# Optimization experiments

Measured on AMD Instinct MI355X. Metric: run time of the kernel, lower is better.

The kernel has to match this reference:

```python
import math
import jax, jax.numpy as jnp
import numpy as np

B, H, L = 8, 512, 4096
N = 64 // 2  # d_state//2 complex pairs
DT_MIN, DT_MAX = 1e-3, 0.1


def setup_inputs() -> dict:
    key = jax.random.key(0)
    k_u, k_dt, k_C, k_D, k_W = jax.random.split(key, 5)
    u = jax.random.normal(k_u, (B, H, L), dtype=jnp.float32)
    log_dt = jax.random.uniform(k_dt, (H,), dtype=jnp.float32) * (
        math.log(DT_MAX) - math.log(DT_MIN)) + math.log(DT_MIN)
    log_A_real = jnp.log(0.5 * jnp.ones((H, N), dtype=jnp.float32))
    A_imag = math.pi * jnp.broadcast_to(jnp.arange(N, dtype=jnp.float32), (H, N))
    C = jax.random.normal(k_C, (H, N, 2), dtype=jnp.float32)  # view_as_real of cfloat
    D = jax.random.normal(k_D, (H,), dtype=jnp.float32)
    W_out = jax.random.normal(k_W, (2 * H, H), dtype=jnp.float32) * 0.05  # 1x1 conv weight
    b_out = jnp.zeros((2 * H,), dtype=jnp.float32)
    return {"u": u, "log_dt": log_dt, "log_A_real": log_A_real, "A_imag": A_imag,
            "C": C, "D": D, "W_out": W_out, "b_out": b_out}


def _ssm_kernel(log_dt, log_A_real, A_imag, C, length):
    dt = jnp.exp(log_dt)                             # (H,)
    A = -jnp.exp(log_A_real) + 1j * A_imag           # (H,N) complex
    dtA = A * dt[:, None]                            # (H,N)
    l = jnp.arange(length, dtype=jnp.float32)
    K = jnp.exp(dtA[:, :, None] * l)                 # (H,N,L) complex Vandermonde
    Cc = C[..., 0] + 1j * C[..., 1]                  # (H,N)
    Cs = Cc * (jnp.exp(dtA) - 1.0) / A               # (H,N)
    return 2.0 * jnp.einsum('hn,hnl->hl', Cs, K).real  # (H,L) real kernel


def reference(u, log_dt, log_A_real, A_imag, C, D, W_out, b_out):
    length = u.shape[-1]
    k = _ssm_kernel(log_dt, log_A_real, A_imag, C, length)  # (H,L)
    n_fft = 2 * length
    k_f = jnp.fft.rfft(k, n=n_fft)                   # (H, L+1)
    u_f = jnp.fft.rfft(u, n=n_fft)                   # (B,H,L+1)
    y = jnp.fft.irfft(u_f * k_f, n=n_fft)[..., :length]  # FFT convolution
    y = y + u * D[:, None]                           # D skip connection
    y = jax.nn.gelu(y, approximate=False)            # torch nn.GELU = exact erf
    y = jnp.einsum('oh,bhl->bol', W_out, y) + b_out[:, None]  # 1x1 conv
    a, b = jnp.split(y, 2, axis=-2)                  # GLU over channel dim
    return a * jax.nn.sigmoid(b)
```

## Files before the change

kernel.cpp:

```cpp
#include <hip/hip_runtime.h>
#include <math.h>

constexpr int cB = 8, cH = 512, cL = 4096, cN = 32;
constexpr int cG = 32, cLC = 128;
constexpr int cHN = cH * cN;

constexpr size_t OF_RR  = 0;
constexpr size_t OF_RI  = (size_t)cHN;
constexpr size_t OF_RPR = (size_t)2*cHN;
constexpr size_t OF_RPI = (size_t)3*cHN;
constexpr size_t OF_C2R = (size_t)4*cHN;
constexpr size_t OF_C2I = (size_t)5*cHN;
constexpr size_t OF_DR  = (size_t)6*cHN;
constexpr size_t OF_DI  = (size_t)7*cHN;
constexpr size_t OF_K   = (size_t)8*cHN;
constexpr size_t OF_WP  = OF_K + (size_t)512*128;
constexpr size_t OF_A   = OF_WP + (size_t)1024*512/2;
constexpr size_t OF_V   = OF_A + (size_t)512*128*192/2;
constexpr size_t OF_XP  = OF_V + (size_t)512*64*128/2;
constexpr size_t OF_G   = OF_XP + (size_t)512*256*64/2;
constexpr size_t OF_GT  = OF_A;

typedef __bf16 bf16x8 __attribute__((ext_vector_type(8)));
typedef float  f32x4  __attribute__((ext_vector_type(4)));

static __device__ __forceinline__ ushort f2bf(float x) {
    unsigned u = __float_as_uint(x);
    unsigned r = (u + 0x7fffu + ((u >> 16) & 1u)) >> 16;
    return (ushort)r;
}
static __device__ __forceinline__ float bf2f(ushort v) {
    return __uint_as_float(((unsigned)v) << 16);
}
static __device__ __forceinline__ unsigned pk2(float a, float b) {
    return (unsigned)f2bf(a) | ((unsigned)f2bf(b) << 16);
}
static __device__ __forceinline__ float gelu(float v) {
    return 0.5f * v * (1.0f + erff(v * 0.70710678118654752f));
}
static __device__ __forceinline__ void gload16(const void* g, void* l) {
    __builtin_amdgcn_global_load_lds(
        (const __attribute__((address_space(1))) unsigned*)g,
        (__attribute__((address_space(3))) unsigned*)l, 16, 0, 0);
}

__global__ void k_consts_vmat(const float* __restrict__ log_dt,
                              const float* __restrict__ log_A_real,
                              const float* __restrict__ A_imag,
                              const float* __restrict__ Cin,
                              float* __restrict__ ws,
                              ushort* __restrict__ wsu)
{
    int tid = blockIdx.x * 256 + threadIdx.x;
    if (tid >= cHN) return;
    int h = tid >> 5, n = tid & 31;
    float dt = expf(log_dt[h]);
    float Ar = -expf(log_A_real[tid]);
    float Ai = A_imag[tid];
    float dr = dt * Ar, di = dt * Ai;
    float er = expf(dr);
    float rr = er * cosf(di), ri = er * sinf(di);
    float erL = expf(dr * (float)cLC);
    float diL = di * (float)cLC;
    float rpr = erL * cosf(diL), rpi = erL * sinf(diL);
    float cr = Cin[2*tid], ci = Cin[2*tid+1];
    float nr = rr - 1.0f, ni = ri;
    float inv = 1.0f / (Ar*Ar + Ai*Ai);
    float wr = (nr*Ar + ni*Ai) * inv;
    float wi = (ni*Ar - nr*Ai) * inv;
    float csr = cr*wr - ci*wi;
    float csi = cr*wi + ci*wr;
    ws[OF_RR  + tid] = rr;  ws[OF_RI  + tid] = ri;
    ws[OF_RPR + tid] = rpr; ws[OF_RPI + tid] = rpi;
    ws[OF_C2R + tid] = 2.0f*csr; ws[OF_C2I + tid] = 2.0f*csi;
    ws[OF_DR  + tid] = dr;  ws[OF_DI  + tid] = di;

    float e127 = expf(dr * 127.f), a127 = di * 127.f;
    float pr = e127 * cosf(a127), pi_ = e127 * sinf(a127);
    float rie = expf(-dr);
    float rc = rie * cosf(di), rs = -rie * sinf(di);
    ushort* vre = wsu + 2*OF_V + ((size_t)h*64 + n) * 128;
    ushort* vim = wsu + 2*OF_V + ((size_t)h*64 + 32 + n) * 128;
    for (int j4 = 0; j4 < 128; j4 += 4) {
        ushort4 r4, i4;
        #pragma unroll
        for (int e = 0; e < 4; ++e) {
            ((ushort*)&r4)[e] = f2bf(pr);
            ((ushort*)&i4)[e] = f2bf(pi_);
            float npr = pr*rc - pi_*rs;
            float npi = pr*rs + pi_*rc;
            pr = npr; pi_ = npi;
        }
        *(ushort4*)&vre[j4] = r4;
        *(ushort4*)&vim[j4] = i4;
    }
}

__global__ void k_pack_w(const float* __restrict__ W, ushort* __restrict__ Wp)
{
    int idx = blockIdx.x * 256 + threadIdx.x;
    int base = idx * 4;
    int m = base >> 9;
    int k = base & 511;
    int src = (m & 1) ? (512 + (m >> 1)) : (m >> 1);
    float4 v = *(const float4*)&W[(size_t)src * 512 + k];
    ushort4 o;
    o.x = f2bf(v.x); o.y = f2bf(v.y); o.z = f2bf(v.z); o.w = f2bf(v.w);
    *(ushort4*)&Wp[base] = o;
}

__global__ void k_embt(const float* __restrict__ ws, const float* __restrict__ Dvec,
                       ushort* __restrict__ wsu)
{
    __shared__ float kv[256];
    int t = threadIdx.x;
    int tid = blockIdx.x * 256 + t;
    int h = tid >> 7, l = tid & 127;
    float fl = (float)l, fl1 = (float)(l + 1);
    const float* dr_ = ws + OF_DR + (size_t)h*32;
    const float* di_ = ws + OF_DI + (size_t)h*32;
    const float* c2r_ = ws + OF_C2R + (size_t)h*32;
    const float* c2i_ = ws + OF_C2I + (size_t)h*32;
    ushort* rowA = wsu + 2*OF_A + ((size_t)h*128 + l) * 192;
    float kacc = 0.f;
    for (int n4 = 0; n4 < 32; n4 += 4) {
        ushort4 prq, npq;
        #pragma unroll
        for (int e = 0; e < 4; ++e) {
            int n = n4 + e;
            float dr = dr_[n], di = di_[n], c2r = c2r_[n], c2i = c2i_[n];
            float e0 = expf(dr * fl), a0 = di * fl;
            float c0 = cosf(a0), s0 = sinf(a0);
            kacc += e0 * (c2r*c0 - c2i*s0);
            float e1 = expf(dr * fl1), a1 = di * fl1;
            float c1 = cosf(a1), s1 = sinf(a1);
            ((ushort*)&prq)[e] = f2bf(e1 * (c2r*c1 - c2i*s1));
            ((ushort*)&npq)[e] = f2bf(-e1 * (c2r*s1 + c2i*c1));
        }
        *(ushort4*)&rowA[128 + n4] = prq;
        *(ushort4*)&rowA[160 + n4] = npq;
    }
    kv[t] = kacc;
    __syncthreads();
    const float* krow = kv + ((t >> 7) << 7);
    float Dh = Dvec[h];
    for (int j8 = 0; j8 < 128; j8 += 8) {
        uint4 q;
        unsigned w[4];
        #pragma unroll
        for (int p = 0; p < 4; ++p) {
            int j0 = j8 + 2*p, j1 = j0 + 1;
            float v0 = (j0 <= l) ? krow[l - j0] : 0.f;
            float v1 = (j1 <= l) ? krow[l - j1] : 0.f;
            if (j0 == l) v0 += Dh;
            if (j1 == l) v1 += Dh;
            w[p] = pk2(v0, v1);
        }
        q.x = w[0]; q.y = w[1]; q.z = w[2]; q.w = w[3];
        *(uint4*)&rowA[j8] = q;
    }
}

__global__ __launch_bounds__(512) void k_conv(const float* __restrict__ u,
                                              const float* __restrict__ ws,
                                              const ushort* __restrict__ wsu,
                                              ushort* __restrict__ g)
{
    __shared__ ushort As[128 * 200];
    __shared__ ushort Bs[256 * 200];
    const int t = threadIdx.x;
    const int h = blockIdx.x;
    const int wave = t >> 6, lane = t & 63;
    const int wm = wave & 1, wn = wave >> 1;
    const int lm = lane & 15, q = lane >> 4;

    uint4 areg[6];
    const int arow = t >> 2, ac0 = (t & 3) * 48;
    {
        const ushort* Ab = wsu + 2*OF_A + ((size_t)h*128 + arow) * 192 + ac0;
        #pragma unroll
        for (int e = 0; e < 6; ++e) areg[e] = *(const uint4*)&Ab[8*e];
    }
    {
        const int vrow = t >> 3, vc0 = (t & 7) * 16;
        const ushort* vs = wsu + 2*OF_V + ((size_t)h*64 + vrow) * 128 + vc0;
        uint4 v0 = *(const uint4*)&vs[0], v1 = *(const uint4*)&vs[8];
        *(uint4*)&As[vrow*200 + vc0]     = v0;
        *(uint4*)&As[vrow*200 + vc0 + 8] = v1;
    }
    {
        const int gc = t >> 1, half = t & 1;
        const int ub = gc >> 5, uc = gc & 31;
        const float* up = u + ((size_t)(ub*cH + h)) * cL + (size_t)uc*128 + half*64;
        ushort* d = &Bs[gc * 200 + half*64];
        #pragma unroll
        for (int e = 0; e < 8; ++e) {
            float4 f0 = *(const float4*)&up[8*e];
            float4 f1 = *(const float4*)&up[8*e + 4];
            uint4 w;
            w.x = pk2(f0.x, f0.y); w.y = pk2(f0.z, f0.w);
            w.z = pk2(f1.x, f1.y); w.w = pk2(f1.z, f1.w);
            *(uint4*)&d[8*e] = w;
        }
    }
    __syncthreads();

    {
        f32x4 accs[4][2];
        #pragma unroll
        for (int i = 0; i < 4; ++i)
            #pragma unroll
            for (int j = 0; j < 2; ++j) accs[i][j] = (f32x4){0.f,0.f,0.f,0.f};
        #pragma unroll
        for (int j0 = 0; j0 < 128; j0 += 32) {
            bf16x8 vf[4], uf[2];
            #pragma unroll
            for (int mi = 0; mi < 4; ++mi)
                vf[mi] = *(const bf16x8*)&As[(16*mi + lm) * 200 + j0 + 8*q];
            #pragma unroll
            for (int ni = 0; ni < 2; ++ni)
                uf[ni] = *(const bf16x8*)&Bs[(32*wave + 16*ni + lm) * 200 + j0 + 8*q];
            #pragma unroll
            for (int mi = 0; mi < 4; ++mi)
                #pragma unroll
                for (int ni = 0; ni < 2; ++ni)
                    accs[mi][ni] = __builtin_amdgcn_mfma_f32_16x16x32_bf16(vf[mi], uf[ni], accs[mi][ni], 0,0,0);
        }
        #pragma unroll
        for (int mi = 0; mi < 4; ++mi)
            #pragma unroll
            for (int ni = 0; ni < 2; ++ni) {
                int col = 32*wave + 16*ni + lm;
                ushort4 st;
                st.x = f2bf(accs[mi][ni][0]); st.y = f2bf(accs[mi][ni][1]);
                st.z = f2bf(accs[mi][ni][2]); st.w = f2bf(accs[mi][ni][3]);
                *(ushort4*)&Bs[col*200 + 128 + 16*mi + 4*q] = st;
            }
    }
    __syncthreads();

    if (t < 256) {
        const int sb = t >> 5, sn = t & 31;
        float rpr = ws[OF_RPR + (size_t)h*32 + sn];
        float rpi = ws[OF_RPI + (size_t)h*32 + sn];
        float Xr = 0.f, Xi = 0.f;
        ushort* p = &Bs[(sb*32) * 200 + 128 + sn];
        #pragma unroll 4
        for (int c = 0; c < cG; ++c, p += 200) {
            float sr = bf2f(p[0]), si = bf2f(p[32]);
            p[0]  = f2bf(Xr);
            p[32] = f2bf(Xi);
            float nXr = fmaf(rpr, Xr, fmaf(-rpi, Xi, sr));
            float nXi = fmaf(rpr, Xi, fmaf(rpi, Xr, si));
            Xr = nXr; Xi = nXi;
        }
    }
    {
        ushort* d = &As[arow*200 + ac0];
        #pragma unroll
        for (int e = 0; e < 6; ++e) *(uint4*)&d[8*e] = areg[e];
    }
    __syncthreads();

    f32x4 acc[4][4];
    #pragma unroll
    for (int i = 0; i < 4; ++i)
        #pragma unroll
        for (int j = 0; j < 4; ++j) acc[i][j] = (f32x4){0.f,0.f,0.f,0.f};

    #pragma unroll
    for (int k0 = 0; k0 < 192; k0 += 32) {
        if ((wm == 0) && (k0 == 64 || k0 == 96)) continue;
        bf16x8 af[4], bfr[4];
        #pragma unroll
        for (int mi = 0; mi < 4; ++mi)
            af[mi] = *(const bf16x8*)&As[(64*wm + 16*mi + lm) * 200 + k0 + 8*q];
        #pragma unroll
        for (int ni = 0; ni < 4; ++ni)
            bfr[ni] = *(const bf16x8*)&Bs[(64*wn + 16*ni + lm) * 200 + k0 + 8*q];
        #pragma unroll
        for (int mi = 0; mi < 4; ++mi)
            #pragma unroll
            for (int ni = 0; ni < 4; ++ni)
                acc[mi][ni] = __builtin_amdgcn_mfma_f32_16x16x32_bf16(af[mi], bfr[ni], acc[mi][ni], 0,0,0);
    }
    #pragma unroll
    for (int ni = 0; ni < 4; ++ni) {
        int gc = 64*wn + 16*ni + lm;
        int ob = gc >> 5, oc = gc & 31;
        ushort* grow = g + ((size_t)(ob*cH + h)) * cL + (size_t)oc*128;
        #pragma unroll
        for (int mi = 0; mi < 4; ++mi) {
            int l = 64*wm + 16*mi + 4*q;
            ushort4 st;
            st.x = f2bf(gelu(acc[mi][ni][0]));
            st.y = f2bf(gelu(acc[mi][ni][1]));
            st.z = f2bf(gelu(acc[mi][ni][2]));
            st.w = f2bf(gelu(acc[mi][ni][3]));
            *(ushort4*)&grow[l] = st;
        }
    }
}

__global__ __launch_bounds__(256) void k_transpose(const ushort* __restrict__ gsrc,
                                                   ushort* __restrict__ gT)
{
    __shared__ ushort tile[64 * 64];
    const int t = threadIdx.x;
    const int b  = blockIdx.z;
    const int h0 = blockIdx.y << 6;
    const int l0 = blockIdx.x << 6;
    const ushort* gb = gsrc + ((size_t)b * cH + h0) * cL + l0;
    const int lb = t & 7;
    #pragma unroll
    for (int half = 0; half < 2; ++half) {
        int r = (t >> 3) + half * 32;
        uint4 v = *(const uint4*)&gb[(size_t)r * cL + lb * 8];
        int sb = lb ^ (r & 7) ^ (r >> 3);
        *(uint4*)&tile[r * 64 + sb * 8] = v;
    }
    __syncthreads();
    ushort* gTb = gT + ((size_t)b * cL + l0) * cH + h0;
    #pragma unroll
    for (int half = 0; half < 2; ++half) {
        int l  = (t >> 3) + half * 32;
        int hb = t & 7;
        ushort vals[8];
        #pragma unroll
        for (int e = 0; e < 8; ++e) {
            int r  = hb * 8 + e;
            int sb = (l >> 3) ^ (r & 7) ^ (r >> 3);
            vals[e] = tile[r * 64 + sb * 8 + (l & 7)];
        }
        *(uint4*)&gTb[(size_t)l * cH + hb * 8] = *(uint4*)vals;
    }
}

__global__ __launch_bounds__(256) void k_gemm2(const ushort* __restrict__ Wp,
                                               const float* __restrict__ bias,
                                               const ushort* __restrict__ gT,
                                               float* __restrict__ out)
{
    __shared__ ushort As[2][128 * 32];
    __shared__ ushort Bs[2][128 * 32];
    const int t    = threadIdx.x;
    const int l0   = blockIdx.x * 128;
    const int by   = blockIdx.y;
    const int b    = blockIdx.z;
    const int wave = t >> 6, lane = t & 63;
    const int wm   = wave & 1, wn = wave >> 1;
    const int lm   = lane & 15, q = lane >> 4;

    const int srow = lane >> 2;
    const int scol = (lane & 3) * 8;
    const ushort* Ag = Wp + (size_t)(by * 128) * 512;
    const ushort* Bg = gT + ((size_t)b * cL + l0) * 512;

    f32x4 acc[4][4];
    #pragma unroll
    for (int i = 0; i < 4; ++i)
        #pragma unroll
        for (int j = 0; j < 4; ++j)
            acc[i][j] = (f32x4){0.f, 0.f, 0.f, 0.f};

    auto stage = [&](ushort* Asb, ushort* Bsb, int k0) {
        #pragma unroll
        for (int j = 0; j < 2; ++j) {
            int row = 32*wave + 16*j + srow;
            gload16(Ag + (size_t)row * 512 + k0 + scol,
                    (char*)Asb + wave*2048 + j*1024);
            gload16(Bg + (size_t)row * 512 + k0 + scol,
                    (char*)Bsb + wave*2048 + j*1024);
        }
    };
    auto compute = [&](const ushort* Asb, const ushort* Bsb) {
        bf16x8 af[4], bfr[4];
        #pragma unroll
        for (int mi = 0; mi < 4; ++mi)
            af[mi] = *(const bf16x8*)&Asb[(64*wm + 16*mi + lm) * 32 + 8*q];
        #pragma unroll
        for (int ni = 0; ni < 4; ++ni)
            bfr[ni] = *(const bf16x8*)&Bsb[(64*wn + 16*ni + lm) * 32 + 8*q];
        #pragma unroll
        for (int mi = 0; mi < 4; ++mi)
            #pragma unroll
            for (int ni = 0; ni < 4; ++ni)
                acc[mi][ni] = __builtin_amdgcn_mfma_f32_16x16x32_bf16(af[mi], bfr[ni], acc[mi][ni], 0,0,0);
    };

    stage(As[0], Bs[0], 0);
    __syncthreads();
    int cur = 0;
    for (int ks = 0; ks < 15; ++ks) {
        stage(As[cur ^ 1], Bs[cur ^ 1], (ks + 1) * 32);
        compute(As[cur], Bs[cur]);
        __syncthreads();
        cur ^= 1;
    }
    compute(As[cur], Bs[cur]);

    const int obase = by * 64 + 32 * wm;
    #pragma unroll
    for (int mi = 0; mi < 4; ++mi) {
        #pragma unroll
        for (int p = 0; p < 2; ++p) {
            int o = obase + 8*mi + 2*q + p;
            float ba = bias[o], bb = bias[512 + o];
            float* orow = out + ((size_t)b * cH + o) * cL + l0 + 64*wn + lm;
            #pragma unroll
            for (int ni = 0; ni < 4; ++ni) {
                float av = acc[mi][ni][2*p]     + ba;
                float gv = acc[mi][ni][2*p + 1] + bb;
                orow[16 * ni] = av / (1.f + expf(-gv));
            }
        }
    }
}

extern "C" void kernel_launch(void* const* d_in, const int* in_sizes, int n_in,
                              void* d_out, int out_size, void* d_ws, size_t ws_size,
                              hipStream_t stream)
{
    (void)in_sizes; (void)n_in; (void)out_size; (void)ws_size;
    const float* u          = (const float*)d_in[0];
    const float* log_dt     = (const float*)d_in[1];
    const float* log_A_real = (const float*)d_in[2];
    const float* A_imag     = (const float*)d_in[3];
    const float* C          = (const float*)d_in[4];
    const float* D          = (const float*)d_in[5];
    const float* W          = (const float*)d_in[6];
    const float* bias       = (const float*)d_in[7];
    float* out = (float*)d_out;
    float* ws  = (float*)d_ws;
    ushort* wsu = (ushort*)d_ws;
    ushort* Wp  = wsu + 2*OF_WP;
    ushort* gbf = wsu + 2*OF_G;
    ushort* gTu = wsu + 2*OF_GT;

    hipLaunchKernelGGL(k_consts_vmat, dim3(cHN/256), dim3(256), 0, stream,
                       log_dt, log_A_real, A_imag, C, ws, wsu);
    hipLaunchKernelGGL(k_pack_w, dim3(1024*512/4/256), dim3(256), 0, stream, W, Wp);
    hipLaunchKernelGGL(k_embt, dim3(512*128/256), dim3(256), 0, stream, ws, D, wsu);
    hipLaunchKernelGGL(k_conv, dim3(512), dim3(512), 0, stream, u, ws, wsu, gbf);
    hipLaunchKernelGGL(k_transpose, dim3(cL/64, cH/64, cB), dim3(256), 0, stream, gbf, gTu);
    hipLaunchKernelGGL(k_gemm2, dim3(cL/128, 1024/128, cB), dim3(256), 0, stream,
                       Wp, bias, gTu, out);
}
```

Measured before the change: 267.2 us.

## Double k_conv block to 1024 threads and stage output through LDS

k_conv now runs 16 waves per block instead of 8, halving each wave's MFMA tile in both the intra-chunk GEMM and the chunk-output GEMM, and splitting the global loads across more threads. The GELU results are first written into a padded shared-memory tile and then stored to global memory as contiguous 16-byte vectors, replacing scattered 8-byte stores. This aims for more latency hiding and better-coalesced writes. It costs extra barriers, and the single block per CU (LDS at about 150KB) means one synchronisation stall can leave the whole CU idle.

```diff
diff --git a/kernel.cpp b/kernel.cpp
--- a/kernel.cpp
+++ b/kernel.cpp
@@ -161,40 +161,40 @@
     }
 }
 
-__global__ __launch_bounds__(512) void k_conv(const float* __restrict__ u,
-                                              const float* __restrict__ ws,
-                                              const ushort* __restrict__ wsu,
-                                              ushort* __restrict__ g)
-{
-    __shared__ ushort As[128 * 200];
-    __shared__ ushort Bs[256 * 200];
+__global__ __launch_bounds__(1024) void k_conv(const float* __restrict__ u,
+                                               const float* __restrict__ ws,
+                                               const ushort* __restrict__ wsu,
+                                               ushort* __restrict__ g)
+{
+    __shared__ ushort sh[76800];
+    ushort* As = sh;
+    ushort* Bs = sh + 25600;
+    ushort* Os = sh;
+
     const int t = threadIdx.x;
     const int h = blockIdx.x;
     const int wave = t >> 6, lane = t & 63;
-    const int wm = wave & 1, wn = wave >> 1;
     const int lm = lane & 15, q = lane >> 4;
 
-    uint4 areg[6];
-    const int arow = t >> 2, ac0 = (t & 3) * 48;
+    uint4 areg[3];
+    const int arow = t >> 3, ac0 = (t & 7) * 24;
     {
         const ushort* Ab = wsu + 2*OF_A + ((size_t)h*128 + arow) * 192 + ac0;
         #pragma unroll
-        for (int e = 0; e < 6; ++e) areg[e] = *(const uint4*)&Ab[8*e];
-    }
-    {
-        const int vrow = t >> 3, vc0 = (t & 7) * 16;
-        const ushort* vs = wsu + 2*OF_V + ((size_t)h*64 + vrow) * 128 + vc0;
-        uint4 v0 = *(const uint4*)&vs[0], v1 = *(const uint4*)&vs[8];
-        *(uint4*)&As[vrow*200 + vc0]     = v0;
-        *(uint4*)&As[vrow*200 + vc0 + 8] = v1;
-    }
-    {
-        const int gc = t >> 1, half = t & 1;
+        for (int e = 0; e < 3; ++e) areg[e] = *(const uint4*)&Ab[8*e];
+    }
+    {
+        const int vrow = t >> 4, vc0 = (t & 15) * 8;
+        *(uint4*)&As[vrow*200 + vc0] =
+            *(const uint4*)(wsu + 2*OF_V + ((size_t)h*64 + vrow) * 128 + vc0);
+    }
+    {
+        const int gc = t >> 2, qt = t & 3;
         const int ub = gc >> 5, uc = gc & 31;
-        const float* up = u + ((size_t)(ub*cH + h)) * cL + (size_t)uc*128 + half*64;
-        ushort* d = &Bs[gc * 200 + half*64];
-        #pragma unroll
-        for (int e = 0; e < 8; ++e) {
+        const float* up = u + ((size_t)(ub*cH + h)) * cL + (size_t)uc*128 + qt*32;
+        ushort* d = &Bs[gc * 200 + qt*32];
+        #pragma unroll
+        for (int e = 0; e < 4; ++e) {
             float4 f0 = *(const float4*)&up[8*e];
             float4 f1 = *(const float4*)&up[8*e + 4];
             uint4 w;
@@ -206,36 +206,28 @@
     __syncthreads();
 
     {
-        f32x4 accs[4][2];
-        #pragma unroll
-        for (int i = 0; i < 4; ++i)
-            #pragma unroll
-            for (int j = 0; j < 2; ++j) accs[i][j] = (f32x4){0.f,0.f,0.f,0.f};
+        f32x4 accs[4];
+        #pragma unroll
+        for (int i = 0; i < 4; ++i) accs[i] = (f32x4){0.f,0.f,0.f,0.f};
         #pragma unroll
         for (int j0 = 0; j0 < 128; j0 += 32) {
-            bf16x8 vf[4], uf[2];
+            bf16x8 vf[4], uf;
             #pragma unroll
             for (int mi = 0; mi < 4; ++mi)
                 vf[mi] = *(const bf16x8*)&As[(16*mi + lm) * 200 + j0 + 8*q];
-            #pragma unroll
-            for (int ni = 0; ni < 2; ++ni)
-                uf[ni] = *(const bf16x8*)&Bs[(32*wave + 16*ni + lm) * 200 + j0 + 8*q];
+            uf = *(const bf16x8*)&Bs[(16*wave + lm) * 200 + j0 + 8*q];
             #pragma unroll
             for (int mi = 0; mi < 4; ++mi)
-                #pragma unroll
-                for (int ni = 0; ni < 2; ++ni)
-                    accs[mi][ni] = __builtin_amdgcn_mfma_f32_16x16x32_bf16(vf[mi], uf[ni], accs[mi][ni], 0,0,0);
-        }
-        #pragma unroll
-        for (int mi = 0; mi < 4; ++mi)
-            #pragma unroll
-            for (int ni = 0; ni < 2; ++ni) {
-                int col = 32*wave + 16*ni + lm;
-                ushort4 st;
-                st.x = f2bf(accs[mi][ni][0]); st.y = f2bf(accs[mi][ni][1]);
-                st.z = f2bf(accs[mi][ni][2]); st.w = f2bf(accs[mi][ni][3]);
-                *(ushort4*)&Bs[col*200 + 128 + 16*mi + 4*q] = st;
-            }
+                accs[mi] = __builtin_amdgcn_mfma_f32_16x16x32_bf16(vf[mi], uf, accs[mi], 0,0,0);
+        }
+        const int col = 16*wave + lm;
+        #pragma unroll
+        for (int mi = 0; mi < 4; ++mi) {
+            ushort4 st;
+            st.x = f2bf(accs[mi][0]); st.y = f2bf(accs[mi][1]);
+            st.z = f2bf(accs[mi][2]); st.w = f2bf(accs[mi][3]);
+            *(ushort4*)&Bs[col*200 + 128 + 16*mi + 4*q] = st;
+        }
     }
     __syncthreads();
 
@@ -258,37 +250,38 @@
     {
         ushort* d = &As[arow*200 + ac0];
         #pragma unroll
-        for (int e = 0; e < 6; ++e) *(uint4*)&d[8*e] = areg[e];
-    }
-    __syncthreads();
-
-    f32x4 acc[4][4];
+        for (int e = 0; e < 3; ++e) *(uint4*)&d[8*e] = areg[e];
+    }
+    __syncthreads();
+
+    const int wm = wave & 1, wn = wave >> 1;
+    f32x4 acc[4][2];
     #pragma unroll
     for (int i = 0; i < 4; ++i)
         #pragma unroll
-        for (int j = 0; j < 4; ++j) acc[i][j] = (f32x4){0.f,0.f,0.f,0.f};
+        for (int j = 0; j < 2; ++j) acc[i][j] = (f32x4){0.f,0.f,0.f,0.f};
 
     #pragma unroll
     for (int k0 = 0; k0 < 192; k0 += 32) {
         if ((wm == 0) && (k0 == 64 || k0 == 96)) continue;
-        bf16x8 af[4], bfr[4];
+        bf16x8 af[4], bfr[2];
         #pragma unroll
         for (int mi = 0; mi < 4; ++mi)
             af[mi] = *(const bf16x8*)&As[(64*wm + 16*mi + lm) * 200 + k0 + 8*q];
         #pragma unroll
-        for (int ni = 0; ni < 4; ++ni)
-            bfr[ni] = *(const bf16x8*)&Bs[(64*wn + 16*ni + lm) * 200 + k0 + 8*q];
+        for (int ni = 0; ni < 2; ++ni)
+            bfr[ni] = *(const bf16x8*)&Bs[(32*wn + 16*ni + lm) * 200 + k0 + 8*q];
         #pragma unroll
         for (int mi = 0; mi < 4; ++mi)
             #pragma unroll
-            for (int ni = 0; ni < 4; ++ni)
+            for (int ni = 0; ni < 2; ++ni)
                 acc[mi][ni] = __builtin_amdgcn_mfma_f32_16x16x32_bf16(af[mi], bfr[ni], acc[mi][ni], 0,0,0);
     }
-    #pragma unroll
-    for (int ni = 0; ni < 4; ++ni) {
-        int gc = 64*wn + 16*ni + lm;
-        int ob = gc >> 5, oc = gc & 31;
-        ushort* grow = g + ((size_t)(ob*cH + h)) * cL + (size_t)oc*128;
+    __syncthreads();
+
+    #pragma unroll
+    for (int ni = 0; ni < 2; ++ni) {
+        int gc = 32*wn + 16*ni + lm;
         #pragma unroll
         for (int mi = 0; mi < 4; ++mi) {
             int l = 64*wm + 16*mi + 4*q;
@@ -297,8 +290,18 @@
             st.y = f2bf(gelu(acc[mi][ni][1]));
             st.z = f2bf(gelu(acc[mi][ni][2]));
             st.w = f2bf(gelu(acc[mi][ni][3]));
-            *(ushort4*)&grow[l] = st;
-        }
+            *(ushort4*)&Os[gc*136 + l] = st;
+        }
+    }
+    __syncthreads();
+    {
+        const int gc = t >> 2, qt = t & 3;
+        const int ob = gc >> 5, oc = gc & 31;
+        ushort* grow = g + ((size_t)(ob*cH + h)) * cL + (size_t)oc*128 + qt*32;
+        const ushort* s = &Os[gc*136 + qt*32];
+        #pragma unroll
+        for (int e = 0; e < 4; ++e)
+            *(uint4*)&grow[8*e] = *(const uint4*)&s[8*e];
     }
 }
 
@@ -441,7 +444,7 @@
                        log_dt, log_A_real, A_imag, C, ws, wsu);
     hipLaunchKernelGGL(k_pack_w, dim3(1024*512/4/256), dim3(256), 0, stream, W, Wp);
     hipLaunchKernelGGL(k_embt, dim3(512*128/256), dim3(256), 0, stream, ws, D, wsu);
-    hipLaunchKernelGGL(k_conv, dim3(512), dim3(512), 0, stream, u, ws, wsu, gbf);
+    hipLaunchKernelGGL(k_conv, dim3(512), dim3(1024), 0, stream, u, ws, wsu, gbf);
     hipLaunchKernelGGL(k_transpose, dim3(cL/64, cH/64, cB), dim3(256), 0, stream, gbf, gTu);
     hipLaunchKernelGGL(k_gemm2, dim3(cL/128, 1024/128, cB), dim3(256), 0, stream,
                        Wp, bias, gTu, out);
```

Result: no change. 263.1 us (-1.6%).

## Split conv kernel across batch pairs and stage GELU output through LDS

Applied to the files above, without the earlier changes.

k_conv now runs on a 4x512 grid, each block covering two batches of one channel instead of all eight. This shrinks the Bs shared buffer fourfold, so more blocks fit per CU, and gives four times as many blocks to spread across CUs. The GELU outputs are first written to LDS and then stored to global memory as contiguous 16-element rows, so writes are coalesced. The cost is that every block reloads the per-channel A and V matrices, which repeats global reads, and the launch bound hint limits registers per thread.

```diff
diff --git a/kernel.cpp b/kernel.cpp
--- a/kernel.cpp
+++ b/kernel.cpp
@@ -161,17 +161,17 @@
     }
 }
 
-__global__ __launch_bounds__(512) void k_conv(const float* __restrict__ u,
-                                              const float* __restrict__ ws,
-                                              const ushort* __restrict__ wsu,
-                                              ushort* __restrict__ g)
+__global__ __launch_bounds__(512, 4) void k_conv(const float* __restrict__ u,
+                                                 const float* __restrict__ ws,
+                                                 const ushort* __restrict__ wsu,
+                                                 ushort* __restrict__ g)
 {
     __shared__ ushort As[128 * 200];
-    __shared__ ushort Bs[256 * 200];
+    __shared__ ushort Bs[64 * 200];
     const int t = threadIdx.x;
-    const int h = blockIdx.x;
+    const int bh = blockIdx.x;
+    const int h  = blockIdx.y;
     const int wave = t >> 6, lane = t & 63;
-    const int wm = wave & 1, wn = wave >> 1;
     const int lm = lane & 15, q = lane >> 4;
 
     uint4 areg[6];
@@ -189,57 +189,49 @@
         *(uint4*)&As[vrow*200 + vc0 + 8] = v1;
     }
     {
-        const int gc = t >> 1, half = t & 1;
-        const int ub = gc >> 5, uc = gc & 31;
-        const float* up = u + ((size_t)(ub*cH + h)) * cL + (size_t)uc*128 + half*64;
-        ushort* d = &Bs[gc * 200 + half*64];
-        #pragma unroll
-        for (int e = 0; e < 8; ++e) {
-            float4 f0 = *(const float4*)&up[8*e];
-            float4 f1 = *(const float4*)&up[8*e + 4];
-            uint4 w;
-            w.x = pk2(f0.x, f0.y); w.y = pk2(f0.z, f0.w);
-            w.z = pk2(f1.x, f1.y); w.w = pk2(f1.z, f1.w);
-            *(uint4*)&d[8*e] = w;
-        }
-    }
-    __syncthreads();
-
-    {
-        f32x4 accs[4][2];
-        #pragma unroll
-        for (int i = 0; i < 4; ++i)
+        const int gc = t >> 3, seg = t & 7;
+        const int b = 2*bh + (gc >> 5), uc = gc & 31;
+        const float* up = u + ((size_t)(b*cH + h)) * cL + (size_t)uc*128 + seg*16;
+        float4 f0 = *(const float4*)&up[0],  f1 = *(const float4*)&up[4];
+        float4 f2 = *(const float4*)&up[8],  f3 = *(const float4*)&up[12];
+        uint4 w0, w1;
+        w0.x = pk2(f0.x,f0.y); w0.y = pk2(f0.z,f0.w);
+        w0.z = pk2(f1.x,f1.y); w0.w = pk2(f1.z,f1.w);
+        w1.x = pk2(f2.x,f2.y); w1.y = pk2(f2.z,f2.w);
+        w1.z = pk2(f3.x,f3.y); w1.w = pk2(f3.z,f3.w);
+        ushort* d = &Bs[gc * 200 + seg*16];
+        *(uint4*)&d[0] = w0; *(uint4*)&d[8] = w1;
+    }
+    __syncthreads();
+
+    {
+        const int tile = wave & 3, mi_b = (wave >> 2) * 2;
+        f32x4 accs[2];
+        #pragma unroll
+        for (int i = 0; i < 2; ++i) accs[i] = (f32x4){0.f,0.f,0.f,0.f};
+        #pragma unroll
+        for (int j0 = 0; j0 < 128; j0 += 32) {
+            bf16x8 vf[2], uf;
             #pragma unroll
-            for (int j = 0; j < 2; ++j) accs[i][j] = (f32x4){0.f,0.f,0.f,0.f};
-        #pragma unroll
-        for (int j0 = 0; j0 < 128; j0 += 32) {
-            bf16x8 vf[4], uf[2];
+            for (int i = 0; i < 2; ++i)
+                vf[i] = *(const bf16x8*)&As[(16*(mi_b+i) + lm) * 200 + j0 + 8*q];
+            uf = *(const bf16x8*)&Bs[(16*tile + lm) * 200 + j0 + 8*q];
             #pragma unroll
-            for (int mi = 0; mi < 4; ++mi)
-                vf[mi] = *(const bf16x8*)&As[(16*mi + lm) * 200 + j0 + 8*q];
-            #pragma unroll
-            for (int ni = 0; ni < 2; ++ni)
-                uf[ni] = *(const bf16x8*)&Bs[(32*wave + 16*ni + lm) * 200 + j0 + 8*q];
-            #pragma unroll
-            for (int mi = 0; mi < 4; ++mi)
-                #pragma unroll
-                for (int ni = 0; ni < 2; ++ni)
-                    accs[mi][ni] = __builtin_amdgcn_mfma_f32_16x16x32_bf16(vf[mi], uf[ni], accs[mi][ni], 0,0,0);
-        }
-        #pragma unroll
-        for (int mi = 0; mi < 4; ++mi)
-            #pragma unroll
-            for (int ni = 0; ni < 2; ++ni) {
-                int col = 32*wave + 16*ni + lm;
-                ushort4 st;
-                st.x = f2bf(accs[mi][ni][0]); st.y = f2bf(accs[mi][ni][1]);
-                st.z = f2bf(accs[mi][ni][2]); st.w = f2bf(accs[mi][ni][3]);
-                *(ushort4*)&Bs[col*200 + 128 + 16*mi + 4*q] = st;
-            }
-    }
-    __syncthreads();
-
-    if (t < 256) {
+            for (int i = 0; i < 2; ++i)
+                accs[i] = __builtin_amdgcn_mfma_f32_16x16x32_bf16(vf[i], uf, accs[i], 0,0,0);
+        }
+        const int col = 16*tile + lm;
+        #pragma unroll
+        for (int i = 0; i < 2; ++i) {
+            ushort4 st;
+            st.x = f2bf(accs[i][0]); st.y = f2bf(accs[i][1]);
+            st.z = f2bf(accs[i][2]); st.w = f2bf(accs[i][3]);
+            *(ushort4*)&Bs[col*200 + 128 + 16*(mi_b+i) + 4*q] = st;
+        }
+    }
+    __syncthreads();
+
+    if (t < 64) {
         const int sb = t >> 5, sn = t & 31;
         float rpr = ws[OF_RPR + (size_t)h*32 + sn];
         float rpi = ws[OF_RPI + (size_t)h*32 + sn];
@@ -262,43 +254,47 @@
     }
     __syncthreads();
 
-    f32x4 acc[4][4];
-    #pragma unroll
-    for (int i = 0; i < 4; ++i)
-        #pragma unroll
-        for (int j = 0; j < 4; ++j) acc[i][j] = (f32x4){0.f,0.f,0.f,0.f};
+    const int wm = wave & 1, wn = wave >> 1;
+    f32x4 acc[4];
+    #pragma unroll
+    for (int i = 0; i < 4; ++i) acc[i] = (f32x4){0.f,0.f,0.f,0.f};
 
     #pragma unroll
     for (int k0 = 0; k0 < 192; k0 += 32) {
         if ((wm == 0) && (k0 == 64 || k0 == 96)) continue;
-        bf16x8 af[4], bfr[4];
+        bf16x8 af[4], bfr;
         #pragma unroll
         for (int mi = 0; mi < 4; ++mi)
             af[mi] = *(const bf16x8*)&As[(64*wm + 16*mi + lm) * 200 + k0 + 8*q];
-        #pragma unroll
-        for (int ni = 0; ni < 4; ++ni)
-            bfr[ni] = *(const bf16x8*)&Bs[(64*wn + 16*ni + lm) * 200 + k0 + 8*q];
+        bfr = *(const bf16x8*)&Bs[(16*wn + lm) * 200 + k0 + 8*q];
         #pragma unroll
         for (int mi = 0; mi < 4; ++mi)
-            #pragma unroll
-            for (int ni = 0; ni < 4; ++ni)
-                acc[mi][ni] = __builtin_amdgcn_mfma_f32_16x16x32_bf16(af[mi], bfr[ni], acc[mi][ni], 0,0,0);
-    }
-    #pragma unroll
-    for (int ni = 0; ni < 4; ++ni) {
-        int gc = 64*wn + 16*ni + lm;
-        int ob = gc >> 5, oc = gc & 31;
-        ushort* grow = g + ((size_t)(ob*cH + h)) * cL + (size_t)oc*128;
+            acc[mi] = __builtin_amdgcn_mfma_f32_16x16x32_bf16(af[mi], bfr, acc[mi], 0,0,0);
+    }
+    __syncthreads();
+
+    ushort* Os = Bs;
+    {
+        int gc = 16*wn + lm;
         #pragma unroll
         for (int mi = 0; mi < 4; ++mi) {
             int l = 64*wm + 16*mi + 4*q;
             ushort4 st;
-            st.x = f2bf(gelu(acc[mi][ni][0]));
-            st.y = f2bf(gelu(acc[mi][ni][1]));
-            st.z = f2bf(gelu(acc[mi][ni][2]));
-            st.w = f2bf(gelu(acc[mi][ni][3]));
-            *(ushort4*)&grow[l] = st;
-        }
+            st.x = f2bf(gelu(acc[mi][0]));
+            st.y = f2bf(gelu(acc[mi][1]));
+            st.z = f2bf(gelu(acc[mi][2]));
+            st.w = f2bf(gelu(acc[mi][3]));
+            *(ushort4*)&Os[gc*136 + l] = st;
+        }
+    }
+    __syncthreads();
+    {
+        const int gc = t >> 3, seg = t & 7;
+        const int b = 2*bh + (gc >> 5), oc = gc & 31;
+        ushort* grow = g + ((size_t)(b*cH + h)) * cL + (size_t)oc*128 + seg*16;
+        const ushort* s = &Os[gc*136 + seg*16];
+        *(uint4*)&grow[0] = *(const uint4*)&s[0];
+        *(uint4*)&grow[8] = *(const uint4*)&s[8];
     }
 }
 
@@ -441,7 +437,7 @@
                        log_dt, log_A_real, A_imag, C, ws, wsu);
     hipLaunchKernelGGL(k_pack_w, dim3(1024*512/4/256), dim3(256), 0, stream, W, Wp);
     hipLaunchKernelGGL(k_embt, dim3(512*128/256), dim3(256), 0, stream, ws, D, wsu);
-    hipLaunchKernelGGL(k_conv, dim3(512), dim3(512), 0, stream, u, ws, wsu, gbf);
+    hipLaunchKernelGGL(k_conv, dim3(4, 512), dim3(512), 0, stream, u, ws, wsu, gbf);
     hipLaunchKernelGGL(k_transpose, dim3(cL/64, cH/64, cB), dim3(256), 0, stream, gbf, gTu);
     hipLaunchKernelGGL(k_gemm2, dim3(cL/128, 1024/128, cB), dim3(256), 0, stream,
                        Wp, bias, gTu, out);
```

Result: slower. 275.4 us (+3.1%).
